# Kernel optimization log

Hardware: AMD Instinct MI355X
Metric: run time of the kernel (lower is better)

The kernel has to match this reference:

```python
import jax, jax.numpy as jnp
import numpy as np

B, S, D = 4, 2048, 768
H, R = 12, 8
Dh = D // H


def setup_inputs() -> dict:
    key = jax.random.key(0)
    ks = jax.random.split(key, 12)
    s_in = 1.0 / np.sqrt(D)
    s_r = 1.0 / np.sqrt(R)
    return {
        "x": jax.random.normal(ks[0], (B, S, D), jnp.float32),
        "Wq0": jax.random.normal(ks[1], (D, D), jnp.float32) * s_in,
        "Aq": jax.random.normal(ks[2], (D, R), jnp.float32) * s_in,
        "Bq": jax.random.normal(ks[3], (R, D), jnp.float32) * s_r,
        "Wk0": jax.random.normal(ks[4], (D, D), jnp.float32) * s_in,
        "Ak": jax.random.normal(ks[5], (D, R), jnp.float32) * s_in,
        "Bk": jax.random.normal(ks[6], (R, D), jnp.float32) * s_r,
        "Wv0": jax.random.normal(ks[7], (D, D), jnp.float32) * s_in,
        "Av": jax.random.normal(ks[8], (D, R), jnp.float32) * s_in,
        "Bv": jax.random.normal(ks[9], (R, D), jnp.float32) * s_r,
        "Wo": jax.random.normal(ks[10], (D, D), jnp.float32) * s_in,
        "bo": jnp.zeros((D,), jnp.float32),
    }


def _lora(x, W0, A, Bm):
    # x @ W0 + (x @ A) @ B  -- low-rank adapter on frozen W0
    return x @ W0 + (x @ A) @ Bm


def _split_heads(t):
    # [B,S,D] -> [B,H,S,Dh]
    return t.reshape(B, S, H, Dh).transpose(0, 2, 1, 3)


def reference(x, Wq0, Aq, Bq, Wk0, Ak, Bk, Wv0, Av, Bv, Wo, bo):
    q = _split_heads(_lora(x, Wq0, Aq, Bq))
    k = _split_heads(_lora(x, Wk0, Ak, Bk))
    v = _split_heads(_lora(x, Wv0, Av, Bv))
    scale = 1.0 / jnp.sqrt(jnp.asarray(Dh, x.dtype))
    scores = jnp.einsum("bhqd,bhkd->bhqk", q, k) * scale  # [B,H,S,S]
    weights = jax.nn.softmax(scores, axis=-1)
    attn = jnp.einsum("bhqk,bhkd->bhqd", weights, v)
    concat = attn.transpose(0, 2, 1, 3).reshape(B, S, D)
    return concat @ Wo + bo
```

## Files before the change

### kernel.cpp

```cpp
#include <hip/hip_runtime.h>
#include <hip/hip_bf16.h>


typedef unsigned short ushort_t;
typedef __bf16 bf16x8 __attribute__((ext_vector_type(8)));
typedef float f32x4 __attribute__((ext_vector_type(4)));
typedef unsigned short ushort8 __attribute__((ext_vector_type(8)));
typedef __attribute__((address_space(1))) unsigned int gu32;
typedef __attribute__((address_space(3))) unsigned int lu32;

__device__ __forceinline__ unsigned short f2bf(float f) {
  unsigned int u = __builtin_bit_cast(unsigned int, f);
  u += 0x7fffu + ((u >> 16) & 1u);
  return (unsigned short)(u >> 16);
}

__device__ __forceinline__ void gld_lds16(const void* g, void* s) {
  __builtin_amdgcn_global_load_lds((gu32*)(unsigned long long)g,
                                   (lu32*)(unsigned int)(unsigned long long)s,
                                   16, 0, 0);
}

__device__ __forceinline__ f32x4 mfma16(bf16x8 a, bf16x8 b, f32x4 c) {
  return __builtin_amdgcn_mfma_f32_16x16x32_bf16(a, b, c, 0, 0, 0);
}

__global__ __launch_bounds__(256) void prep_weights(
    const float* __restrict__ Wq0, const float* __restrict__ Aq, const float* __restrict__ Bq,
    const float* __restrict__ Wk0, const float* __restrict__ Ak, const float* __restrict__ Bk,
    const float* __restrict__ Wv0, const float* __restrict__ Av, const float* __restrict__ Bv,
    const float* __restrict__ Wo,
    ushort_t* __restrict__ WeffT, ushort_t* __restrict__ WoT)
{
  __shared__ float tile[32][33];
  __shared__ float tA[32][8];
  __shared__ float tB[8][32];
  const int mat = blockIdx.y;
  const int kt = blockIdx.x / 24, nt = blockIdx.x % 24;
  const int k0 = kt * 32, n0 = nt * 32;
  const float* W0 = (mat == 0) ? Wq0 : (mat == 1) ? Wk0 : (mat == 2) ? Wv0 : Wo;
  const float* Am = (mat == 0) ? Aq : (mat == 1) ? Ak : (mat == 2) ? Av : nullptr;
  const float* Bm = (mat == 0) ? Bq : (mat == 1) ? Bk : (mat == 2) ? Bv : nullptr;
  const int tid = threadIdx.x;
#pragma unroll
  for (int i = 0; i < 4; i++) {
    int rr = i * 8 + (tid >> 5), c = tid & 31;
    tile[rr][c] = W0[(k0 + rr) * 768 + n0 + c];
  }
  if (Am) {
    tA[tid >> 3][tid & 7] = Am[(k0 + (tid >> 3)) * 8 + (tid & 7)];
    tB[tid >> 5][tid & 31] = Bm[(tid >> 5) * 768 + n0 + (tid & 31)];
  }
  __syncthreads();
#pragma unroll
  for (int i = 0; i < 4; i++) {
    int kk = tid & 31;
    int nn = i * 8 + (tid >> 5);
    float val = tile[kk][nn];
    if (Am) {
#pragma unroll
      for (int rr = 0; rr < 8; rr++) val += tA[kk][rr] * tB[rr][nn];
    }
    int n = n0 + nn, kg = k0 + kk;
    if (mat < 3) WeffT[((long)mat * 768 + n) * 768 + kg] = f2bf(val);
    else         WoT[(long)n * 768 + kg] = f2bf(val);
  }
}

__global__ __launch_bounds__(256) void cast_x(const float* __restrict__ x,
                                              ushort_t* __restrict__ xb)
{
  long i = (long)blockIdx.x * 256 + threadIdx.x;
  const float4* xp = (const float4*)x;
  float4 a = xp[i * 2], c = xp[i * 2 + 1];
  ushort8 rv;
  rv[0] = f2bf(a.x); rv[1] = f2bf(a.y); rv[2] = f2bf(a.z); rv[3] = f2bf(a.w);
  rv[4] = f2bf(c.x); rv[5] = f2bf(c.y); rv[6] = f2bf(c.z); rv[7] = f2bf(c.w);
  *(ushort8*)&xb[i * 8] = rv;
}

template <int MODE>
__global__ __launch_bounds__(256) void gemm_bt(
    const ushort_t* __restrict__ A, const ushort_t* __restrict__ Bt,
    ushort_t* __restrict__ q, ushort_t* __restrict__ kbuf, ushort_t* __restrict__ v,
    float* __restrict__ out, const float* __restrict__ bo)
{
  constexpr int K = 768;
  __shared__ ushort_t As[128 * 64];
  __shared__ ushort_t Bs[128 * 64];
  const int tid = threadIdx.x;
  const int l = tid & 63, w = tid >> 6;
  const int wm = w >> 1, wn = w & 1;
  const int lr = l & 15, lg = l >> 4;
  const long rowBase = (long)blockIdx.x * 128;
  const long colBase = (long)blockIdx.y * 128;
  f32x4 acc[4][4] = {};

  for (int k0 = 0; k0 < K; k0 += 64) {
    __syncthreads();
#pragma unroll
    for (int i = 0; i < 4; i++) {
      int ci = i * 256 + tid;
      gld_lds16(A + (rowBase + (ci >> 3)) * K + k0 + (ci & 7) * 8, &As[ci * 8]);
    }
#pragma unroll
    for (int i = 0; i < 4; i++) {
      int ci = i * 256 + tid;
      gld_lds16(Bt + (colBase + (ci >> 3)) * K + k0 + (ci & 7) * 8, &Bs[ci * 8]);
    }
    asm volatile("s_waitcnt vmcnt(0)" ::: "memory");
    __syncthreads();
#pragma unroll
    for (int ks = 0; ks < 2; ks++) {
      bf16x8 af[4], bf[4];
#pragma unroll
      for (int m = 0; m < 4; m++)
        af[m] = *(const bf16x8*)&As[(wm * 64 + m * 16 + lr) * 64 + ks * 32 + lg * 8];
#pragma unroll
      for (int n = 0; n < 4; n++)
        bf[n] = *(const bf16x8*)&Bs[(wn * 64 + n * 16 + lr) * 64 + ks * 32 + lg * 8];
#pragma unroll
      for (int m = 0; m < 4; m++)
#pragma unroll
        for (int n = 0; n < 4; n++)
          acc[m][n] = mfma16(af[m], bf[n], acc[m][n]);
    }
  }

  if (MODE == 0) {
    const int mat = (int)(colBase / 768);
    ushort_t* dst = (mat == 0) ? q : (mat == 1) ? kbuf : v;
    const float scl = (mat == 0) ? 0.125f * 1.4426950408889634f : 1.0f;
    const long cb = colBase - (long)mat * 768;
#pragma unroll
    for (int m = 0; m < 4; m++)
#pragma unroll
      for (int n = 0; n < 4; n++) {
        long col = cb + wn * 64 + n * 16 + lr;
#pragma unroll
        for (int r = 0; r < 4; r++) {
          long row = rowBase + wm * 64 + m * 16 + lg * 4 + r;
          dst[row * 768 + col] = f2bf(acc[m][n][r] * scl);
        }
      }
  } else {
#pragma unroll
    for (int m = 0; m < 4; m++)
#pragma unroll
      for (int n = 0; n < 4; n++) {
        long col = colBase + wn * 64 + n * 16 + lr;
        float bv = bo[col];
#pragma unroll
        for (int r = 0; r < 4; r++) {
          long row = rowBase + wm * 64 + m * 16 + lg * 4 + r;
          out[row * 768 + col] = acc[m][n][r] + bv;
        }
      }
  }
}

__global__ __launch_bounds__(256) void transpose_v(const ushort_t* __restrict__ V,
                                                   ushort_t* __restrict__ Vt)
{
  __shared__ ushort_t t[64][65];
  const int tid = threadIdx.x;
  const int s0 = blockIdx.x * 64;
  const int bh = blockIdx.y;
  const int b = bh / 12, h = bh % 12;
#pragma unroll
  for (int it = 0; it < 2; it++) {
    int r = it * 32 + (tid >> 3), c8 = tid & 7;
    ushort8 val = *(const ushort8*)&V[((long)(b * 2048 + s0 + r)) * 768 + h * 64 + c8 * 8];
#pragma unroll
    for (int j = 0; j < 8; j++) t[c8 * 8 + j][r] = val[j];
  }
  __syncthreads();
#pragma unroll
  for (int it = 0; it < 2; it++) {
    int d = it * 32 + (tid >> 3), k8 = tid & 7;
    ushort8 val;
#pragma unroll
    for (int j = 0; j < 8; j++) val[j] = t[d][k8 * 8 + j];
    *(ushort8*)&Vt[((long)bh * 64 + d) * 2048 + s0 + k8 * 8] = val;
  }
}

__global__ __launch_bounds__(256) void attn_fwd(
    const ushort_t* __restrict__ Q, const ushort_t* __restrict__ Kg,
    const ushort_t* __restrict__ VtG, ushort_t* __restrict__ O)
{
  constexpr int D = 768, S = 2048;
  __shared__ ushort_t Ks[64 * 64];
  __shared__ ushort_t Vs[64 * 64];
  __shared__ ushort_t Ps[4][32 * 72];
  const int tid = threadIdx.x;
  const int l = tid & 63, w = tid >> 6;
  const int lr = l & 15, lg = l >> 4;
  const int i = blockIdx.x;
  const int xcd = i & 7, j = i >> 3;
  const int bh = xcd * 6 + (j >> 4);
  const int q0 = (j & 15) * 128;
  const int b = bh / 12, h = bh % 12;
  const ushort_t* Qb = Q + (long)b * S * D + h * 64;
  const ushort_t* Kb = Kg + (long)b * S * D + h * 64;
  const ushort_t* Vb = VtG + (long)bh * 64 * S;

  bf16x8 qf[2][2];
#pragma unroll
  for (int m = 0; m < 2; m++)
#pragma unroll
    for (int ks = 0; ks < 2; ks++)
      qf[m][ks] = *(const bf16x8*)&Qb[(long)(q0 + w * 32 + m * 16 + lr) * D + ks * 32 + lg * 8];

  bf16x8 ones;
#pragma unroll
  for (int e = 0; e < 8; e++) ones[e] = (__bf16)1.0f;

  f32x4 o[2][4], o1[2];
#pragma unroll
  for (int m = 0; m < 2; m++) {
    o1[m] = (f32x4){0.f, 0.f, 0.f, 0.f};
#pragma unroll
    for (int n = 0; n < 4; n++) o[m][n] = (f32x4){0.f, 0.f, 0.f, 0.f};
  }

  const int swz = lr & 7;

  for (int kt = 0; kt < 32; kt++) {
    const int kbase = kt * 64;
    __syncthreads();
#pragma unroll
    for (int it = 0; it < 2; it++) {
      int ci = it * 256 + tid;
      int r = ci >> 3, bp = ci & 7;
      gld_lds16(Kb + (long)(kbase + r) * D + ((bp ^ (r & 7)) * 8), &Ks[ci * 8]);
    }
#pragma unroll
    for (int it = 0; it < 2; it++) {
      int ci = it * 256 + tid;
      int d = ci >> 3, bp = ci & 7;
      gld_lds16(Vb + (long)d * S + kbase + ((bp ^ (d & 7)) * 8), &Vs[ci * 8]);
    }
    asm volatile("s_waitcnt vmcnt(0)" ::: "memory");
    __syncthreads();

    f32x4 s[2][4];
#pragma unroll
    for (int m = 0; m < 2; m++)
#pragma unroll
      for (int n = 0; n < 4; n++) s[m][n] = (f32x4){0.f, 0.f, 0.f, 0.f};
#pragma unroll
    for (int ks = 0; ks < 2; ks++) {
#pragma unroll
      for (int n = 0; n < 4; n++) {
        int key = n * 16 + lr;
        bf16x8 kf = *(const bf16x8*)&Ks[key * 64 + (((ks * 4 + lg) ^ swz) * 8)];
#pragma unroll
        for (int m = 0; m < 2; m++)
          s[m][n] = mfma16(qf[m][ks], kf, s[m][n]);
      }
    }
#pragma unroll
    for (int m = 0; m < 2; m++)
#pragma unroll
      for (int n = 0; n < 4; n++)
#pragma unroll
        for (int r = 0; r < 4; r++) {
          float p = __builtin_amdgcn_exp2f(s[m][n][r]);
          Ps[w][(m * 16 + lg * 4 + r) * 72 + n * 16 + lr] = f2bf(p);
        }
#pragma unroll
    for (int ks = 0; ks < 2; ks++) {
      bf16x8 pf[2], vf[4];
#pragma unroll
      for (int m = 0; m < 2; m++)
        pf[m] = *(const bf16x8*)&Ps[w][(m * 16 + lr) * 72 + ks * 32 + lg * 8];
#pragma unroll
      for (int n = 0; n < 4; n++) {
        int d = n * 16 + lr;
        vf[n] = *(const bf16x8*)&Vs[d * 64 + (((ks * 4 + lg) ^ swz) * 8)];
      }
#pragma unroll
      for (int m = 0; m < 2; m++) {
        o1[m] = mfma16(pf[m], ones, o1[m]);
#pragma unroll
        for (int n = 0; n < 4; n++)
          o[m][n] = mfma16(pf[m], vf[n], o[m][n]);
      }
    }
  }
#pragma unroll
  for (int m = 0; m < 2; m++) {
    float inv[4];
#pragma unroll
    for (int r = 0; r < 4; r++) inv[r] = 1.0f / o1[m][r];
#pragma unroll
    for (int n = 0; n < 4; n++)
#pragma unroll
      for (int r = 0; r < 4; r++) {
        float val = o[m][n][r] * inv[r];
        O[((long)b * S + q0 + w * 32 + m * 16 + lg * 4 + r) * D + h * 64 + n * 16 + lr] = f2bf(val);
      }
  }
}

extern "C" void kernel_launch(void* const* d_in, const int* in_sizes, int n_in,
                              void* d_out, int out_size, void* d_ws, size_t ws_size,
                              hipStream_t stream)
{
  const float* x   = (const float*)d_in[0];
  const float* Wq0 = (const float*)d_in[1];
  const float* Aq  = (const float*)d_in[2];
  const float* Bq  = (const float*)d_in[3];
  const float* Wk0 = (const float*)d_in[4];
  const float* Ak  = (const float*)d_in[5];
  const float* Bk  = (const float*)d_in[6];
  const float* Wv0 = (const float*)d_in[7];
  const float* Av  = (const float*)d_in[8];
  const float* Bv  = (const float*)d_in[9];
  const float* Wo  = (const float*)d_in[10];
  const float* bo  = (const float*)d_in[11];
  float* out = (float*)d_out;

  char* ws = (char*)d_ws;
  const long SZ = 8192L * 768 * 2;
  ushort_t* xb    = (ushort_t*)(ws);
  ushort_t* Qb    = (ushort_t*)(ws + SZ);
  ushort_t* Kb    = (ushort_t*)(ws + 2 * SZ);
  ushort_t* Vb    = (ushort_t*)(ws + 3 * SZ);
  ushort_t* At    = (ushort_t*)(ws + 4 * SZ);
  ushort_t* WeffT = (ushort_t*)(ws + 5 * SZ);
  ushort_t* WoT   = (ushort_t*)(ws + 5 * SZ + 2304L * 768 * 2);
  ushort_t* Vt    = xb;

  hipLaunchKernelGGL(prep_weights, dim3(576, 4), dim3(256), 0, stream,
                     Wq0, Aq, Bq, Wk0, Ak, Bk, Wv0, Av, Bv, Wo, WeffT, WoT);
  hipLaunchKernelGGL(cast_x, dim3(3072), dim3(256), 0, stream, x, xb);
  hipLaunchKernelGGL((gemm_bt<0>), dim3(64, 18), dim3(256), 0, stream,
                     xb, WeffT, Qb, Kb, Vb, (float*)nullptr, (const float*)nullptr);
  hipLaunchKernelGGL(transpose_v, dim3(32, 48), dim3(256), 0, stream, Vb, Vt);
  hipLaunchKernelGGL(attn_fwd, dim3(768), dim3(256), 0, stream, Qb, Kb, Vt, At);
  hipLaunchKernelGGL((gemm_bt<1>), dim3(64, 6), dim3(256), 0, stream,
                     At, WoT, (ushort_t*)nullptr, (ushort_t*)nullptr, (ushort_t*)nullptr,
                     out, bo);
}
```

Measured before the change: 181.2 us.

## Double-buffer K/V tiles in attention, fuse V transpose into projection GEMM

The attention kernel now double-buffers K and V tiles in LDS, prefetching the next tile while computing the current one. It uses a partial vmcnt wait and raw barriers, with s_setprio raised around the MFMA blocks. The P scratch buffer drops its padding in favour of an XOR swizzle to avoid LDS bank conflicts. The QKV GEMM epilogue writes V directly in transposed layout with 4-wide packed stores, which removes the separate transpose kernel launch and its extra memory round trip, though the transposed stores are strided in global memory.

```diff
diff --git a/kernel.cpp b/kernel.cpp
--- a/kernel.cpp
+++ b/kernel.cpp
@@ -6,6 +6,7 @@
 typedef __bf16 bf16x8 __attribute__((ext_vector_type(8)));
 typedef float f32x4 __attribute__((ext_vector_type(4)));
 typedef unsigned short ushort8 __attribute__((ext_vector_type(8)));
+typedef unsigned short ushort4_t __attribute__((ext_vector_type(4)));
 typedef __attribute__((address_space(1))) unsigned int gu32;
 typedef __attribute__((address_space(3))) unsigned int lu32;
 
@@ -82,7 +83,7 @@
 template <int MODE>
 __global__ __launch_bounds__(256) void gemm_bt(
     const ushort_t* __restrict__ A, const ushort_t* __restrict__ Bt,
-    ushort_t* __restrict__ q, ushort_t* __restrict__ kbuf, ushort_t* __restrict__ v,
+    ushort_t* __restrict__ q, ushort_t* __restrict__ kbuf, ushort_t* __restrict__ vt,
     float* __restrict__ out, const float* __restrict__ bo)
 {
   constexpr int K = 768;
@@ -129,20 +130,37 @@
 
   if (MODE == 0) {
     const int mat = (int)(colBase / 768);
-    ushort_t* dst = (mat == 0) ? q : (mat == 1) ? kbuf : v;
-    const float scl = (mat == 0) ? 0.125f * 1.4426950408889634f : 1.0f;
-    const long cb = colBase - (long)mat * 768;
-#pragma unroll
-    for (int m = 0; m < 4; m++)
-#pragma unroll
-      for (int n = 0; n < 4; n++) {
-        long col = cb + wn * 64 + n * 16 + lr;
-#pragma unroll
-        for (int r = 0; r < 4; r++) {
-          long row = rowBase + wm * 64 + m * 16 + lg * 4 + r;
-          dst[row * 768 + col] = f2bf(acc[m][n][r] * scl);
+    if (mat == 2) {
+      const long cb = colBase - 1536;
+#pragma unroll
+      for (int m = 0; m < 4; m++) {
+        long srow = rowBase + wm * 64 + m * 16 + lg * 4;
+        long b = srow >> 11, s = srow & 2047;
+#pragma unroll
+        for (int n = 0; n < 4; n++) {
+          long col = cb + wn * 64 + n * 16 + lr;
+          ushort4_t pk;
+#pragma unroll
+          for (int r = 0; r < 4; r++) pk[r] = f2bf(acc[m][n][r]);
+          *(ushort4_t*)&vt[(b * 768 + col) * 2048 + s] = pk;
         }
       }
+    } else {
+      ushort_t* dst = (mat == 0) ? q : kbuf;
+      const float scl = (mat == 0) ? 0.125f * 1.4426950408889634f : 1.0f;
+      const long cb = colBase - (long)mat * 768;
+#pragma unroll
+      for (int m = 0; m < 4; m++)
+#pragma unroll
+        for (int n = 0; n < 4; n++) {
+          long col = cb + wn * 64 + n * 16 + lr;
+#pragma unroll
+          for (int r = 0; r < 4; r++) {
+            long row = rowBase + wm * 64 + m * 16 + lg * 4 + r;
+            dst[row * 768 + col] = f2bf(acc[m][n][r] * scl);
+          }
+        }
+    }
   } else {
 #pragma unroll
     for (int m = 0; m < 4; m++)
@@ -159,40 +177,14 @@
   }
 }
 
-__global__ __launch_bounds__(256) void transpose_v(const ushort_t* __restrict__ V,
-                                                   ushort_t* __restrict__ Vt)
-{
-  __shared__ ushort_t t[64][65];
-  const int tid = threadIdx.x;
-  const int s0 = blockIdx.x * 64;
-  const int bh = blockIdx.y;
-  const int b = bh / 12, h = bh % 12;
-#pragma unroll
-  for (int it = 0; it < 2; it++) {
-    int r = it * 32 + (tid >> 3), c8 = tid & 7;
-    ushort8 val = *(const ushort8*)&V[((long)(b * 2048 + s0 + r)) * 768 + h * 64 + c8 * 8];
-#pragma unroll
-    for (int j = 0; j < 8; j++) t[c8 * 8 + j][r] = val[j];
-  }
-  __syncthreads();
-#pragma unroll
-  for (int it = 0; it < 2; it++) {
-    int d = it * 32 + (tid >> 3), k8 = tid & 7;
-    ushort8 val;
-#pragma unroll
-    for (int j = 0; j < 8; j++) val[j] = t[d][k8 * 8 + j];
-    *(ushort8*)&Vt[((long)bh * 64 + d) * 2048 + s0 + k8 * 8] = val;
-  }
-}
-
 __global__ __launch_bounds__(256) void attn_fwd(
     const ushort_t* __restrict__ Q, const ushort_t* __restrict__ Kg,
     const ushort_t* __restrict__ VtG, ushort_t* __restrict__ O)
 {
   constexpr int D = 768, S = 2048;
-  __shared__ ushort_t Ks[64 * 64];
-  __shared__ ushort_t Vs[64 * 64];
-  __shared__ ushort_t Ps[4][32 * 72];
+  __shared__ ushort_t Ks[2][64 * 64];
+  __shared__ ushort_t Vs[2][64 * 64];
+  __shared__ ushort_t Ps[4][32 * 64];
   const int tid = threadIdx.x;
   const int l = tid & 63, w = tid >> 6;
   const int lr = l & 15, lg = l >> 4;
@@ -203,7 +195,7 @@
   const int b = bh / 12, h = bh % 12;
   const ushort_t* Qb = Q + (long)b * S * D + h * 64;
   const ushort_t* Kb = Kg + (long)b * S * D + h * 64;
-  const ushort_t* Vb = VtG + (long)bh * 64 * S;
+  const ushort_t* Vb = VtG + ((long)b * 768 + h * 64) * S;
 
   bf16x8 qf[2][2];
 #pragma unroll
@@ -226,40 +218,52 @@
 
   const int swz = lr & 7;
 
-  for (int kt = 0; kt < 32; kt++) {
-    const int kbase = kt * 64;
-    __syncthreads();
+  auto STAGE = [&](int t, int bi) {
+    const int kbase = t * 64;
 #pragma unroll
     for (int it = 0; it < 2; it++) {
       int ci = it * 256 + tid;
       int r = ci >> 3, bp = ci & 7;
-      gld_lds16(Kb + (long)(kbase + r) * D + ((bp ^ (r & 7)) * 8), &Ks[ci * 8]);
+      gld_lds16(Kb + (long)(kbase + r) * D + ((bp ^ (r & 7)) * 8), &Ks[bi][ci * 8]);
     }
 #pragma unroll
     for (int it = 0; it < 2; it++) {
       int ci = it * 256 + tid;
       int d = ci >> 3, bp = ci & 7;
-      gld_lds16(Vb + (long)d * S + kbase + ((bp ^ (d & 7)) * 8), &Vs[ci * 8]);
-    }
-    asm volatile("s_waitcnt vmcnt(0)" ::: "memory");
-    __syncthreads();
+      gld_lds16(Vb + (long)d * S + kbase + ((bp ^ (d & 7)) * 8), &Vs[bi][ci * 8]);
+    }
+  };
+
+  STAGE(0, 0);
+
+  for (int kt = 0; kt < 32; kt++) {
+    const int cur = kt & 1;
+    STAGE((kt + 1) & 31, cur ^ 1);
+    asm volatile("s_waitcnt vmcnt(4)" ::: "memory");
+    __builtin_amdgcn_s_barrier();
+
+    const ushort_t* ksb = &Ks[cur][0];
+    const ushort_t* vsb = &Vs[cur][0];
 
     f32x4 s[2][4];
 #pragma unroll
     for (int m = 0; m < 2; m++)
 #pragma unroll
       for (int n = 0; n < 4; n++) s[m][n] = (f32x4){0.f, 0.f, 0.f, 0.f};
+    __builtin_amdgcn_s_setprio(1);
 #pragma unroll
     for (int ks = 0; ks < 2; ks++) {
 #pragma unroll
       for (int n = 0; n < 4; n++) {
         int key = n * 16 + lr;
-        bf16x8 kf = *(const bf16x8*)&Ks[key * 64 + (((ks * 4 + lg) ^ swz) * 8)];
+        bf16x8 kf = *(const bf16x8*)&ksb[key * 64 + (((ks * 4 + lg) ^ swz) * 8)];
 #pragma unroll
         for (int m = 0; m < 2; m++)
           s[m][n] = mfma16(qf[m][ks], kf, s[m][n]);
       }
     }
+    __builtin_amdgcn_s_setprio(0);
+
 #pragma unroll
     for (int m = 0; m < 2; m++)
 #pragma unroll
@@ -267,19 +271,23 @@
 #pragma unroll
         for (int r = 0; r < 4; r++) {
           float p = __builtin_amdgcn_exp2f(s[m][n][r]);
-          Ps[w][(m * 16 + lg * 4 + r) * 72 + n * 16 + lr] = f2bf(p);
+          int ro = m * 16 + lg * 4 + r;
+          int ch = (n * 2 + (lr >> 3)) ^ ((ro >> 1) & 7);
+          Ps[w][ro * 64 + ch * 8 + (lr & 7)] = f2bf(p);
         }
+
 #pragma unroll
     for (int ks = 0; ks < 2; ks++) {
       bf16x8 pf[2], vf[4];
 #pragma unroll
       for (int m = 0; m < 2; m++)
-        pf[m] = *(const bf16x8*)&Ps[w][(m * 16 + lr) * 72 + ks * 32 + lg * 8];
+        pf[m] = *(const bf16x8*)&Ps[w][(m * 16 + lr) * 64 + (((ks * 4 + lg) ^ ((lr >> 1) & 7)) * 8)];
 #pragma unroll
       for (int n = 0; n < 4; n++) {
         int d = n * 16 + lr;
-        vf[n] = *(const bf16x8*)&Vs[d * 64 + (((ks * 4 + lg) ^ swz) * 8)];
-      }
+        vf[n] = *(const bf16x8*)&vsb[d * 64 + (((ks * 4 + lg) ^ swz) * 8)];
+      }
+      __builtin_amdgcn_s_setprio(1);
 #pragma unroll
       for (int m = 0; m < 2; m++) {
         o1[m] = mfma16(pf[m], ones, o1[m]);
@@ -287,8 +295,13 @@
         for (int n = 0; n < 4; n++)
           o[m][n] = mfma16(pf[m], vf[n], o[m][n]);
       }
-    }
-  }
+      __builtin_amdgcn_s_setprio(0);
+    }
+
+    asm volatile("" ::: "memory");
+    __builtin_amdgcn_s_barrier();
+  }
+
 #pragma unroll
   for (int m = 0; m < 2; m++) {
     float inv[4];
@@ -327,18 +340,16 @@
   ushort_t* xb    = (ushort_t*)(ws);
   ushort_t* Qb    = (ushort_t*)(ws + SZ);
   ushort_t* Kb    = (ushort_t*)(ws + 2 * SZ);
-  ushort_t* Vb    = (ushort_t*)(ws + 3 * SZ);
+  ushort_t* Vt    = (ushort_t*)(ws + 3 * SZ);
   ushort_t* At    = (ushort_t*)(ws + 4 * SZ);
   ushort_t* WeffT = (ushort_t*)(ws + 5 * SZ);
   ushort_t* WoT   = (ushort_t*)(ws + 5 * SZ + 2304L * 768 * 2);
-  ushort_t* Vt    = xb;
 
   hipLaunchKernelGGL(prep_weights, dim3(576, 4), dim3(256), 0, stream,
                      Wq0, Aq, Bq, Wk0, Ak, Bk, Wv0, Av, Bv, Wo, WeffT, WoT);
   hipLaunchKernelGGL(cast_x, dim3(3072), dim3(256), 0, stream, x, xb);
   hipLaunchKernelGGL((gemm_bt<0>), dim3(64, 18), dim3(256), 0, stream,
-                     xb, WeffT, Qb, Kb, Vb, (float*)nullptr, (const float*)nullptr);
-  hipLaunchKernelGGL(transpose_v, dim3(32, 48), dim3(256), 0, stream, Vb, Vt);
+                     xb, WeffT, Qb, Kb, Vt, (float*)nullptr, (const float*)nullptr);
   hipLaunchKernelGGL(attn_fwd, dim3(768), dim3(256), 0, stream, Qb, Kb, Vt, At);
   hipLaunchKernelGGL((gemm_bt<1>), dim3(64, 6), dim3(256), 0, stream,
                      At, WoT, (ushort_t*)nullptr, (ushort_t*)nullptr, (ushort_t*)nullptr,
```

After: 180.1 us. Within noise of the previous version (-0.6%).
